# Kernel tuning notes

Hardware: AMD Instinct MI355X
Metric: run time of the kernel (lower is better)

Reference implementation:

```python
import jax, jax.numpy as jnp
import numpy as np

R = 4          # num_roles
L = 2          # num_layers
DIN = 128      # input/hidden feature dim
DOUT = 40     # output classes
N = 40000      # nodes
E = 480000     # edges


def setup_inputs() -> dict:
    key = jax.random.key(0)
    ks = jax.random.split(key, 12)
    x = jax.random.normal(ks[0], (N, R + DIN), dtype=jnp.float32)
    edge_index = jax.random.randint(ks[1], (2, E), 0, N, dtype=jnp.int64)
    s = 0.05
    Wm = jax.random.normal(ks[2], (L, R, DIN, DIN), dtype=jnp.float32) * s
    bm = jax.random.normal(ks[3], (L, R, DIN), dtype=jnp.float32) * s
    Wa = jax.random.normal(ks[4], (L, R, 2 * DIN, DIN), dtype=jnp.float32) * s
    ba = jax.random.normal(ks[5], (L, R, DIN), dtype=jnp.float32) * s
    W1 = jax.random.normal(ks[6], (DIN, DIN), dtype=jnp.float32) * s
    b1 = jax.random.normal(ks[7], (DIN,), dtype=jnp.float32) * s
    W2 = jax.random.normal(ks[8], (DIN, DOUT), dtype=jnp.float32) * s
    b2 = jax.random.normal(ks[9], (DOUT,), dtype=jnp.float32) * s
    return {"x": x, "edge_index": edge_index, "Wm": Wm, "bm": bm,
            "Wa": Wa, "ba": ba, "W1": W1, "b1": b1, "W2": W2, "b2": b2}


def _role_coef(roles):
    # Faithful to the original loop bug: linears[0] applied twice with roles[:,0],
    # linears[r] with roles[:,r] for r=1..R-2, linears[R-1] unused.
    return jnp.concatenate(
        [2.0 * roles[:, :1], roles[:, 1:R - 1], jnp.zeros_like(roles[:, :1])], axis=1)


def _graphsage_layer(xfull, src, dst, Wm_l, bm_l, Wa_l, ba_l):
    roles = xfull[:, :R]          # [N, R]
    feats = xfull[:, R:]          # [N, D]
    # --- message: gather source nodes, per-role linear + weighted sum, relu ---
    xr = roles[src]               # [E, R]
    xf = feats[src]               # [E, D]
    coef = _role_coef(xr)         # [E, R]
    lin = jnp.einsum('ei,rio->ero', xf, Wm_l) + bm_l[None]   # [E, R, O]
    msg = jax.nn.relu(jnp.einsum('er,ero->eo', coef, lin))    # [E, O]
    # --- aggregate: scatter-mean to target nodes ---
    ssum = jax.ops.segment_sum(msg, dst, num_segments=N)      # [N, O]
    cnt = jax.ops.segment_sum(jnp.ones((msg.shape[0], 1), msg.dtype), dst,
                              num_segments=N)                 # [N, 1]
    aggr = jnp.where(cnt > 0, ssum / jnp.maximum(cnt, 1.0), 0.0)
    # --- update: concat, per-role linear + weighted sum, relu, L2 normalize ---
    cat = jnp.concatenate([feats, aggr], axis=1)              # [N, D+O]
    coefn = _role_coef(roles)                                 # [N, R]
    lin2 = jnp.einsum('ni,rio->nro', cat, Wa_l) + ba_l[None]  # [N, R, O]
    out = jax.nn.relu(jnp.einsum('nr,nro->no', coefn, lin2))  # [N, O]
    norm = jnp.linalg.norm(out, axis=1, keepdims=True)
    return out / jnp.maximum(norm, 1e-12)


def reference(x, edge_index, Wm, bm, Wa, ba, W1, b1, W2, b2):
    src = edge_index[0]
    dst = edge_index[1]
    h = x
    for l in range(L):
        feats = _graphsage_layer(h, src, dst, Wm[l], bm[l], Wa[l], ba[l])
        feats = jax.nn.relu(feats)  # extra relu from GNNStack (dropout is identity in eval)
        h = jnp.concatenate([h[:, :R], feats], axis=1)
    z = h[:, R:]
    z = z @ W1 + b1               # post_mp linear 1 (dropout identity)
    logits = z @ W2 + b2          # post_mp linear 2
    return jax.nn.log_softmax(logits, axis=1)
```

## Files before the change

kernel.cpp:

```cpp
#include <hip/hip_runtime.h>
#include <hip/hip_fp16.h>

#define RN 4
#define XSTRIDE 132

typedef float    frag_cd __attribute__((ext_vector_type(4)));
typedef _Float16 frag_h  __attribute__((ext_vector_type(8)));

__global__ void count_kernel(const int* __restrict__ ei, int E, int* __restrict__ cnt) {
    int e = blockIdx.x * 256 + threadIdx.x;
    if (e < E) atomicAdd(&cnt[ei[E + e]], 1);
}

__global__ void scanA(const int* __restrict__ cnt, int N, int* __restrict__ bsums) {
    __shared__ int s[256];
    int t = threadIdx.x, n = blockIdx.x * 256 + t;
    s[t] = (n < N) ? cnt[n] : 0;
    __syncthreads();
    for (int off = 128; off > 0; off >>= 1) {
        if (t < off) s[t] += s[t + off];
        __syncthreads();
    }
    if (t == 0) bsums[blockIdx.x] = s[0];
}

__global__ void scanB(int* __restrict__ bsums, int nb) {
    __shared__ int s[256];
    int t = threadIdx.x;
    int v = (t < nb) ? bsums[t] : 0;
    s[t] = v; __syncthreads();
    for (int off = 1; off < 256; off <<= 1) {
        int add = (t >= off) ? s[t - off] : 0;
        __syncthreads();
        s[t] += add;
        __syncthreads();
    }
    if (t < nb) bsums[t] = s[t] - v;
}

__global__ void scanC(const int* __restrict__ cnt, int N,
                      const int* __restrict__ bsums, int* __restrict__ offs) {
    __shared__ int s[256];
    int t = threadIdx.x, n = blockIdx.x * 256 + t;
    int v = (n < N) ? cnt[n] : 0;
    s[t] = v; __syncthreads();
    for (int off = 1; off < 256; off <<= 1) {
        int add = (t >= off) ? s[t - off] : 0;
        __syncthreads();
        s[t] += add;
        __syncthreads();
    }
    if (n < N) {
        offs[n] = bsums[blockIdx.x] + s[t] - v;
        if (n == N - 1) offs[N] = bsums[blockIdx.x] + s[t];
    }
}

__global__ void fill_kernel(const int* __restrict__ ei, int E,
                            const int* __restrict__ offs, int* __restrict__ fc,
                            int* __restrict__ csr) {
    int e = blockIdx.x * 256 + threadIdx.x;
    if (e < E) {
        int dst = ei[E + e];
        int p = offs[dst] + atomicAdd(&fc[dst], 1);
        csr[p] = ei[e];
    }
}

#define CW_M  (6 * 128 * 128)
#define CW_A  (6 * 128 * 256)
#define CW_1  (128 * 128)
#define CW_2  (48 * 128)
__global__ void conv_all(const float* __restrict__ Wm, const float* __restrict__ Wa,
                         const float* __restrict__ W1, const float* __restrict__ W2,
                         _Float16* __restrict__ WmT, _Float16* __restrict__ WaT,
                         _Float16* __restrict__ W1T, _Float16* __restrict__ W2T) {
    int id = blockIdx.x * 256 + threadIdx.x;
    if (id < CW_M) {
        const int K = 128;
        int per = K * 128;
        int lr = id / per;  int l = lr / 3, r = lr - l * 3;
        int rem = id - lr * per;
        int k = rem >> 7, col = rem & 127;
        WmT[((size_t)lr * 128 + col) * K + k] =
            (_Float16)Wm[(((size_t)l * 4 + r) * K + k) * 128 + col];
    } else if (id < CW_M + CW_A) {
        int j = id - CW_M;
        const int K = 256;
        int per = K * 128;
        int lr = j / per;  int l = lr / 3, r = lr - l * 3;
        int rem = j - lr * per;
        int k = rem >> 7, col = rem & 127;
        WaT[((size_t)lr * 128 + col) * K + k] =
            (_Float16)Wa[(((size_t)l * 4 + r) * K + k) * 128 + col];
    } else if (id < CW_M + CW_A + CW_1) {
        int j = id - CW_M - CW_A;
        int col = j >> 7, k = j & 127;
        W1T[j] = (_Float16)W1[k * 128 + col];
    } else if (id < CW_M + CW_A + CW_1 + CW_2) {
        int j = id - CW_M - CW_A - CW_1;
        int col = j >> 7, k = j & 127;
        W2T[j] = (_Float16)((col < 40) ? W2[k * 40 + col] : 0.0f);
    }
}

__global__ void conv_x(const float* __restrict__ x, _Float16* __restrict__ X, int total) {
    int id = blockIdx.x * 256 + threadIdx.x;
    if (id >= total) return;
    int n = id >> 7, k = id & 127;
    X[id] = (_Float16)x[(size_t)n * XSTRIDE + RN + k];
}

__global__ __launch_bounds__(256) void agg_kernel(
    const int* __restrict__ csr, const int* __restrict__ offs,
    const _Float16* __restrict__ Mb, _Float16* __restrict__ S, int N)
{
    int node = blockIdx.x * 8 + (threadIdx.x >> 5);
    int lane = threadIdx.x & 31;
    if (node >= N) return;
    int lo = offs[node], hi = offs[node + 1];
    const uint2* M2 = (const uint2*)Mb;
    float a0 = 0.f, a1 = 0.f, a2 = 0.f, a3 = 0.f;
    int e = lo;
    for (; e + 3 < hi; e += 4) {
        #pragma unroll
        for (int j = 0; j < 4; ++j) {
            uint2 u = M2[(size_t)csr[e + j] * 32 + lane];
            float2 f0 = __half22float2(*(const __half2*)&u.x);
            float2 f1 = __half22float2(*(const __half2*)&u.y);
            a0 += f0.x; a1 += f0.y; a2 += f1.x; a3 += f1.y;
        }
    }
    for (; e < hi; ++e) {
        uint2 u = M2[(size_t)csr[e] * 32 + lane];
        float2 f0 = __half22float2(*(const __half2*)&u.x);
        float2 f1 = __half22float2(*(const __half2*)&u.y);
        a0 += f0.x; a1 += f0.y; a2 += f1.x; a3 += f1.y;
    }
    float inv = (hi > lo) ? 1.0f / (float)(hi - lo) : 0.0f;
    __half2 h0 = __float22half2_rn(make_float2(a0 * inv, a1 * inv));
    __half2 h1 = __float22half2_rn(make_float2(a2 * inv, a3 * inv));
    uint2 st; st.x = *(const uint*)&h0; st.y = *(const uint*)&h1;
    ((uint2*)S)[(size_t)node * 32 + lane] = st;
}

template<int KV, bool NORM>
__global__ __launch_bounds__(256) void gemm_mfma(
    const float* __restrict__ x,
    const _Float16* __restrict__ Fp,
    const _Float16* __restrict__ Sp,
    const _Float16* __restrict__ W,
    const float* __restrict__ bias,
    _Float16* __restrict__ out)
{
    __shared__ float cc[64][3];
    __shared__ float red[64][4];

    const int tid = threadIdx.x;
    const int n0 = blockIdx.x * 64;
    const int lane = tid & 63;
    const int wv = tid >> 6;
    const int q = lane >> 4;
    const int lb = lane & 15;
    const int w32 = wv * 32;

    if (tid < 64) {
        const float* xr = x + (size_t)(n0 + tid) * XSTRIDE;
        cc[tid][0] = 2.0f * xr[0];
        cc[tid][1] = xr[1];
        cc[tid][2] = xr[2];
    }
    __syncthreads();

    _Float16 ch16[4][3];
    #pragma unroll
    for (int nt = 0; nt < 4; ++nt)
        #pragma unroll
        for (int r = 0; r < 3; ++r)
            ch16[nt][r] = (_Float16)cc[nt * 16 + lb][r];

    frag_cd acc[4][2];
    #pragma unroll
    for (int nt = 0; nt < 4; ++nt)
        #pragma unroll
        for (int ct = 0; ct < 2; ++ct)
            acc[nt][ct] = (frag_cd){0.f, 0.f, 0.f, 0.f};

    size_t wrow[3][2];
    #pragma unroll
    for (int r = 0; r < 3; ++r)
        #pragma unroll
        for (int ct = 0; ct < 2; ++ct)
            wrow[r][ct] = ((size_t)(r * 128 + w32 + ct * 16 + lb)) * KV + q * 8;

    size_t arow[4];
    #pragma unroll
    for (int nt = 0; nt < 4; ++nt)
        arow[nt] = (size_t)(n0 + nt * 16 + lb) * 128 + q * 8;

    const int NCH = KV / 32;
    frag_h aF[3][4], bF[3][6];

    auto loadChunk = [&](int c, int buf) {
        const _Float16* ap; int kofs;
        if (KV == 128 || c < 4) { ap = Fp; kofs = c * 32; }
        else                    { ap = Sp; kofs = (c - 4) * 32; }
        #pragma unroll
        for (int nt = 0; nt < 4; ++nt)
            aF[buf][nt] = *(const frag_h*)(ap + arow[nt] + kofs);
        #pragma unroll
        for (int r = 0; r < 3; ++r)
            #pragma unroll
            for (int ct = 0; ct < 2; ++ct)
                bF[buf][r * 2 + ct] = *(const frag_h*)(W + wrow[r][ct] + c * 32);
    };

    loadChunk(0, 0);
    loadChunk(1, 1);

    #pragma unroll
    for (int ch = 0; ch < NCH; ++ch) {
        if (ch + 2 < NCH) loadChunk(ch + 2, (ch + 2) % 3);
        const int cur = ch % 3;
        #pragma unroll
        for (int r = 0; r < 3; ++r) {
            #pragma unroll
            for (int nt = 0; nt < 4; ++nt) {
                frag_h sa = aF[cur][nt] * ch16[nt][r];
                #pragma unroll
                for (int ct = 0; ct < 2; ++ct)
                    acc[nt][ct] = __builtin_amdgcn_mfma_f32_16x16x32_f16(
                        sa, bF[cur][r * 2 + ct], acc[nt][ct], 0, 0, 0);
            }
        }
    }

    float vv[4][2][4];
    #pragma unroll
    for (int ct = 0; ct < 2; ++ct) {
        int col = w32 + ct * 16 + lb;
        float b0 = bias[col], b1 = bias[128 + col], b2 = bias[256 + col];
        #pragma unroll
        for (int nt = 0; nt < 4; ++nt) {
            #pragma unroll
            for (int rg = 0; rg < 4; ++rg) {
                int row = nt * 16 + q * 4 + rg;
                float v = acc[nt][ct][rg]
                        + cc[row][0] * b0 + cc[row][1] * b1 + cc[row][2] * b2;
                vv[nt][ct][rg] = fmaxf(v, 0.0f);
            }
        }
    }

    if (NORM) {
        #pragma unroll
        for (int nt = 0; nt < 4; ++nt) {
            #pragma unroll
            for (int rg = 0; rg < 4; ++rg) {
                float ss = vv[nt][0][rg] * vv[nt][0][rg] + vv[nt][1][rg] * vv[nt][1][rg];
                #pragma unroll
                for (int m = 1; m < 16; m <<= 1) ss += __shfl_xor(ss, m, 64);
                if (lb == 0) red[nt * 16 + q * 4 + rg][wv] = ss;
            }
        }
        __syncthreads();
        #pragma unroll
        for (int nt = 0; nt < 4; ++nt) {
            #pragma unroll
            for (int rg = 0; rg < 4; ++rg) {
                int row = nt * 16 + q * 4 + rg;
                float t = red[row][0] + red[row][1] + red[row][2] + red[row][3];
                float inv = 1.0f / fmaxf(sqrtf(t), 1e-12f);
                #pragma unroll
                for (int ct = 0; ct < 2; ++ct) {
                    int col = w32 + ct * 16 + lb;
                    out[(size_t)(n0 + row) * 128 + col] = (_Float16)(vv[nt][ct][rg] * inv);
                }
            }
        }
    } else {
        #pragma unroll
        for (int nt = 0; nt < 4; ++nt)
            #pragma unroll
            for (int ct = 0; ct < 2; ++ct)
                #pragma unroll
                for (int rg = 0; rg < 4; ++rg) {
                    int row = nt * 16 + q * 4 + rg;
                    int col = w32 + ct * 16 + lb;
                    out[(size_t)(n0 + row) * 128 + col] = (_Float16)vv[nt][ct][rg];
                }
    }
}

__global__ __launch_bounds__(256) void final_mfma(
    const _Float16* __restrict__ F2,
    const _Float16* __restrict__ W1T,
    const float* __restrict__ b1,
    const _Float16* __restrict__ W2T,
    const float* __restrict__ b2,
    float* __restrict__ out)
{
    __shared__ _Float16 Z[64][136];

    const int tid = threadIdx.x;
    const int n0 = blockIdx.x * 64;
    const int lane = tid & 63;
    const int wv = tid >> 6;
    const int q = lane >> 4;
    const int lb = lane & 15;
    const int w32 = wv * 32;

    frag_cd acc[4][2];
    #pragma unroll
    for (int nt = 0; nt < 4; ++nt)
        #pragma unroll
        for (int ct = 0; ct < 2; ++ct) acc[nt][ct] = (frag_cd){0.f, 0.f, 0.f, 0.f};

    #pragma unroll
    for (int ch = 0; ch < 4; ++ch) {
        frag_h aF[4];
        #pragma unroll
        for (int nt = 0; nt < 4; ++nt)
            aF[nt] = *(const frag_h*)(F2 + (size_t)(n0 + nt * 16 + lb) * 128 + ch * 32 + q * 8);
        #pragma unroll
        for (int ct = 0; ct < 2; ++ct) {
            frag_h bF = *(const frag_h*)(W1T + (size_t)(w32 + ct * 16 + lb) * 128 + ch * 32 + q * 8);
            #pragma unroll
            for (int nt = 0; nt < 4; ++nt)
                acc[nt][ct] = __builtin_amdgcn_mfma_f32_16x16x32_f16(aF[nt], bF, acc[nt][ct], 0, 0, 0);
        }
    }
    #pragma unroll
    for (int ct = 0; ct < 2; ++ct) {
        int col = w32 + ct * 16 + lb;
        float bb = b1[col];
        #pragma unroll
        for (int nt = 0; nt < 4; ++nt)
            #pragma unroll
            for (int rg = 0; rg < 4; ++rg)
                Z[nt * 16 + q * 4 + rg][col] = (_Float16)(acc[nt][ct][rg] + bb);
    }
    __syncthreads();

    frag_cd a2[3];
    #pragma unroll
    for (int ct = 0; ct < 3; ++ct) a2[ct] = (frag_cd){0.f, 0.f, 0.f, 0.f};
    #pragma unroll
    for (int ch = 0; ch < 4; ++ch) {
        frag_h zF = *(const frag_h*)&Z[wv * 16 + lb][ch * 32 + q * 8];
        #pragma unroll
        for (int ct = 0; ct < 3; ++ct) {
            frag_h bF = *(const frag_h*)(W2T + (size_t)(ct * 16 + lb) * 128 + ch * 32 + q * 8);
            a2[ct] = __builtin_amdgcn_mfma_f32_16x16x32_f16(zF, bF, a2[ct], 0, 0, 0);
        }
    }

    float lg[3][4];
    #pragma unroll
    for (int ct = 0; ct < 3; ++ct) {
        int col = ct * 16 + lb;
        bool valid = col < 40;
        float bb = valid ? b2[col] : -1e30f;
        #pragma unroll
        for (int rg = 0; rg < 4; ++rg)
            lg[ct][rg] = valid ? (a2[ct][rg] + bb) : -1e30f;
    }
    #pragma unroll
    for (int rg = 0; rg < 4; ++rg) {
        float mx = fmaxf(fmaxf(lg[0][rg], lg[1][rg]), lg[2][rg]);
        #pragma unroll
        for (int m = 1; m < 16; m <<= 1) mx = fmaxf(mx, __shfl_xor(mx, m, 64));
        float sm = __expf(lg[0][rg] - mx) + __expf(lg[1][rg] - mx) + __expf(lg[2][rg] - mx);
        #pragma unroll
        for (int m = 1; m < 16; m <<= 1) sm += __shfl_xor(sm, m, 64);
        float ls = mx + __logf(sm);
        int row = n0 + wv * 16 + q * 4 + rg;
        #pragma unroll
        for (int ct = 0; ct < 3; ++ct) {
            int col = ct * 16 + lb;
            if (col < 40) out[(size_t)row * 40 + col] = lg[ct][rg] - ls;
        }
    }
}

extern "C" void kernel_launch(void* const* d_in, const int* in_sizes, int n_in,
                              void* d_out, int out_size, void* d_ws, size_t ws_size,
                              hipStream_t stream) {
    const float* x  = (const float*)d_in[0];
    const int*   ei = (const int*)d_in[1];
    const float* Wm = (const float*)d_in[2];
    const float* bm = (const float*)d_in[3];
    const float* Wa = (const float*)d_in[4];
    const float* ba = (const float*)d_in[5];
    const float* W1 = (const float*)d_in[6];
    const float* b1 = (const float*)d_in[7];
    const float* W2 = (const float*)d_in[8];
    const float* b2 = (const float*)d_in[9];
    float* out = (float*)d_out;

    const int N = in_sizes[0] / XSTRIDE;
    const int E = in_sizes[1] / 2;
    const int NB = (N + 255) / 256;
    const size_t P = (size_t)N * 128;

    _Float16* Mb  = (_Float16*)d_ws;
    _Float16* X   = Mb + P;
    _Float16* S   = X + P;
    _Float16* F1  = S + P;
    _Float16* WmT = F1 + P;
    _Float16* WaT = WmT + CW_M;
    _Float16* W1T = WaT + CW_A;
    _Float16* W2T = W1T + CW_1;
    int* cnt   = (int*)(W2T + CW_2);
    int* fc    = cnt + N;
    int* offs  = fc + N;
    int* csr   = offs + N + 1;
    int* bsums = csr + E;

    conv_all<<<(CW_M + CW_A + CW_1 + CW_2 + 255) / 256, 256, 0, stream>>>(
        Wm, Wa, W1, W2, WmT, WaT, W1T, W2T);
    conv_x<<<(N * 128 + 255) / 256, 256, 0, stream>>>(x, X, N * 128);

    hipMemsetAsync(cnt, 0, (size_t)2 * N * sizeof(int), stream);
    count_kernel<<<(E + 255) / 256, 256, 0, stream>>>(ei, E, cnt);
    scanA<<<NB, 256, 0, stream>>>(cnt, N, bsums);
    scanB<<<1, 256, 0, stream>>>(bsums, NB);
    scanC<<<NB, 256, 0, stream>>>(cnt, N, bsums, offs);
    fill_kernel<<<(E + 255) / 256, 256, 0, stream>>>(ei, E, offs, fc, csr);

    const int gblk = N / 64;
    for (int l = 0; l < 2; ++l) {
        const _Float16* fp = (l == 0) ? X : F1;
        _Float16* o = (l == 0) ? F1 : X;

        gemm_mfma<128, false><<<gblk, 256, 0, stream>>>(
            x, fp, nullptr,
            WmT + (size_t)l * 3 * 128 * 128, bm + (size_t)l * 4 * 128, Mb);
        agg_kernel<<<(N + 7) / 8, 256, 0, stream>>>(csr, offs, Mb, S, N);
        gemm_mfma<256, true><<<gblk, 256, 0, stream>>>(
            x, fp, S,
            WaT + (size_t)l * 3 * 128 * 256, ba + (size_t)l * 4 * 128, o);
    }

    final_mfma<<<N / 64, 256, 0, stream>>>(X, W1T, b1, W2T, b2, out);
}
```

Before: 307.5 us.

## Fuse prep kernels, drop scanB, widen agg loads, fully preload K=128 GEMM

Merges weight conversion, x conversion (now vectorised float4->half) and edge counting into a single prep kernel. It drops the separate scanB launch by having each scanC block reduce the preceding block sums itself. The aggregation kernel now uses 16 lanes per node with 16-byte loads instead of 32 lanes with 8-byte loads. The K=128 GEMM loads all fragments up front instead of using a rolling triple buffer. Together these cut launch count and per-load overhead, at the cost of more registers in the GEMM and redundant block-sum reductions in scanC.

```diff
diff --git a/kernel.cpp b/kernel.cpp
--- a/kernel.cpp
+++ b/kernel.cpp
@@ -6,75 +6,21 @@
 
 typedef float    frag_cd __attribute__((ext_vector_type(4)));
 typedef _Float16 frag_h  __attribute__((ext_vector_type(8)));
-
-__global__ void count_kernel(const int* __restrict__ ei, int E, int* __restrict__ cnt) {
-    int e = blockIdx.x * 256 + threadIdx.x;
-    if (e < E) atomicAdd(&cnt[ei[E + e]], 1);
-}
-
-__global__ void scanA(const int* __restrict__ cnt, int N, int* __restrict__ bsums) {
-    __shared__ int s[256];
-    int t = threadIdx.x, n = blockIdx.x * 256 + t;
-    s[t] = (n < N) ? cnt[n] : 0;
-    __syncthreads();
-    for (int off = 128; off > 0; off >>= 1) {
-        if (t < off) s[t] += s[t + off];
-        __syncthreads();
-    }
-    if (t == 0) bsums[blockIdx.x] = s[0];
-}
-
-__global__ void scanB(int* __restrict__ bsums, int nb) {
-    __shared__ int s[256];
-    int t = threadIdx.x;
-    int v = (t < nb) ? bsums[t] : 0;
-    s[t] = v; __syncthreads();
-    for (int off = 1; off < 256; off <<= 1) {
-        int add = (t >= off) ? s[t - off] : 0;
-        __syncthreads();
-        s[t] += add;
-        __syncthreads();
-    }
-    if (t < nb) bsums[t] = s[t] - v;
-}
-
-__global__ void scanC(const int* __restrict__ cnt, int N,
-                      const int* __restrict__ bsums, int* __restrict__ offs) {
-    __shared__ int s[256];
-    int t = threadIdx.x, n = blockIdx.x * 256 + t;
-    int v = (n < N) ? cnt[n] : 0;
-    s[t] = v; __syncthreads();
-    for (int off = 1; off < 256; off <<= 1) {
-        int add = (t >= off) ? s[t - off] : 0;
-        __syncthreads();
-        s[t] += add;
-        __syncthreads();
-    }
-    if (n < N) {
-        offs[n] = bsums[blockIdx.x] + s[t] - v;
-        if (n == N - 1) offs[N] = bsums[blockIdx.x] + s[t];
-    }
-}
-
-__global__ void fill_kernel(const int* __restrict__ ei, int E,
-                            const int* __restrict__ offs, int* __restrict__ fc,
-                            int* __restrict__ csr) {
-    int e = blockIdx.x * 256 + threadIdx.x;
-    if (e < E) {
-        int dst = ei[E + e];
-        int p = offs[dst] + atomicAdd(&fc[dst], 1);
-        csr[p] = ei[e];
-    }
-}
 
 #define CW_M  (6 * 128 * 128)
 #define CW_A  (6 * 128 * 256)
 #define CW_1  (128 * 128)
 #define CW_2  (48 * 128)
-__global__ void conv_all(const float* __restrict__ Wm, const float* __restrict__ Wa,
-                         const float* __restrict__ W1, const float* __restrict__ W2,
-                         _Float16* __restrict__ WmT, _Float16* __restrict__ WaT,
-                         _Float16* __restrict__ W1T, _Float16* __restrict__ W2T) {
+#define CW_TOT (CW_M + CW_A + CW_1 + CW_2)
+
+__global__ void prep_kernel(
+    const float* __restrict__ Wm, const float* __restrict__ Wa,
+    const float* __restrict__ W1, const float* __restrict__ W2,
+    _Float16* __restrict__ WmT, _Float16* __restrict__ WaT,
+    _Float16* __restrict__ W1T, _Float16* __restrict__ W2T,
+    const float* __restrict__ x, _Float16* __restrict__ X,
+    const int* __restrict__ ei, int* __restrict__ cnt, int N, int E)
+{
     int id = blockIdx.x * 256 + threadIdx.x;
     if (id < CW_M) {
         const int K = 128;
@@ -84,64 +30,141 @@
         int k = rem >> 7, col = rem & 127;
         WmT[((size_t)lr * 128 + col) * K + k] =
             (_Float16)Wm[(((size_t)l * 4 + r) * K + k) * 128 + col];
-    } else if (id < CW_M + CW_A) {
-        int j = id - CW_M;
+        return;
+    }
+    id -= CW_M;
+    if (id < CW_A) {
         const int K = 256;
         int per = K * 128;
-        int lr = j / per;  int l = lr / 3, r = lr - l * 3;
-        int rem = j - lr * per;
+        int lr = id / per;  int l = lr / 3, r = lr - l * 3;
+        int rem = id - lr * per;
         int k = rem >> 7, col = rem & 127;
         WaT[((size_t)lr * 128 + col) * K + k] =
             (_Float16)Wa[(((size_t)l * 4 + r) * K + k) * 128 + col];
-    } else if (id < CW_M + CW_A + CW_1) {
-        int j = id - CW_M - CW_A;
-        int col = j >> 7, k = j & 127;
-        W1T[j] = (_Float16)W1[k * 128 + col];
-    } else if (id < CW_M + CW_A + CW_1 + CW_2) {
-        int j = id - CW_M - CW_A - CW_1;
-        int col = j >> 7, k = j & 127;
-        W2T[j] = (_Float16)((col < 40) ? W2[k * 40 + col] : 0.0f);
-    }
-}
-
-__global__ void conv_x(const float* __restrict__ x, _Float16* __restrict__ X, int total) {
-    int id = blockIdx.x * 256 + threadIdx.x;
-    if (id >= total) return;
-    int n = id >> 7, k = id & 127;
-    X[id] = (_Float16)x[(size_t)n * XSTRIDE + RN + k];
+        return;
+    }
+    id -= CW_A;
+    if (id < CW_1) {
+        int col = id >> 7, k = id & 127;
+        W1T[id] = (_Float16)W1[k * 128 + col];
+        return;
+    }
+    id -= CW_1;
+    if (id < CW_2) {
+        int col = id >> 7, k = id & 127;
+        W2T[id] = (_Float16)((col < 40) ? W2[k * 40 + col] : 0.0f);
+        return;
+    }
+    id -= CW_2;
+    if (id < N * 16) {
+        int n = id >> 4, g = id & 15;
+        const float4* src = (const float4*)(x + (size_t)n * XSTRIDE + RN + g * 8);
+        float4 f0 = src[0], f1 = src[1];
+        __half2 h0 = __float22half2_rn(make_float2(f0.x, f0.y));
+        __half2 h1 = __float22half2_rn(make_float2(f0.z, f0.w));
+        __half2 h2 = __float22half2_rn(make_float2(f1.x, f1.y));
+        __half2 h3 = __float22half2_rn(make_float2(f1.z, f1.w));
+        uint4 st; st.x = *(uint*)&h0; st.y = *(uint*)&h1;
+        st.z = *(uint*)&h2; st.w = *(uint*)&h3;
+        ((uint4*)X)[(size_t)n * 16 + g] = st;
+        return;
+    }
+    id -= N * 16;
+    if (id < E) atomicAdd(&cnt[ei[E + id]], 1);
+}
+
+__global__ void scanA(const int* __restrict__ cnt, int N, int* __restrict__ bsums) {
+    __shared__ int s[256];
+    int t = threadIdx.x, n = blockIdx.x * 256 + t;
+    s[t] = (n < N) ? cnt[n] : 0;
+    __syncthreads();
+    for (int off = 128; off > 0; off >>= 1) {
+        if (t < off) s[t] += s[t + off];
+        __syncthreads();
+    }
+    if (t == 0) bsums[blockIdx.x] = s[0];
+}
+
+__global__ void scanC(const int* __restrict__ cnt, int N, int nb,
+                      const int* __restrict__ bsums, int* __restrict__ offs) {
+    __shared__ int s[256];
+    __shared__ int basebuf[256];
+    int t = threadIdx.x, n = blockIdx.x * 256 + t;
+    int bid = blockIdx.x;
+    basebuf[t] = (t < bid && t < nb) ? bsums[t] : 0;
+    __syncthreads();
+    for (int off = 128; off > 0; off >>= 1) {
+        if (t < off) basebuf[t] += basebuf[t + off];
+        __syncthreads();
+    }
+    int base = basebuf[0];
+    int v = (n < N) ? cnt[n] : 0;
+    s[t] = v; __syncthreads();
+    for (int off = 1; off < 256; off <<= 1) {
+        int add = (t >= off) ? s[t - off] : 0;
+        __syncthreads();
+        s[t] += add;
+        __syncthreads();
+    }
+    if (n < N) {
+        offs[n] = base + s[t] - v;
+        if (n == N - 1) offs[N] = base + s[t];
+    }
+}
+
+__global__ void fill_kernel(const int* __restrict__ ei, int E,
+                            const int* __restrict__ offs, int* __restrict__ fc,
+                            int* __restrict__ csr) {
+    int e = blockIdx.x * 256 + threadIdx.x;
+    if (e < E) {
+        int dst = ei[E + e];
+        int p = offs[dst] + atomicAdd(&fc[dst], 1);
+        csr[p] = ei[e];
+    }
 }
 
 __global__ __launch_bounds__(256) void agg_kernel(
     const int* __restrict__ csr, const int* __restrict__ offs,
     const _Float16* __restrict__ Mb, _Float16* __restrict__ S, int N)
 {
-    int node = blockIdx.x * 8 + (threadIdx.x >> 5);
-    int lane = threadIdx.x & 31;
+    int node = blockIdx.x * 16 + (threadIdx.x >> 4);
+    int lane = threadIdx.x & 15;
     if (node >= N) return;
     int lo = offs[node], hi = offs[node + 1];
-    const uint2* M2 = (const uint2*)Mb;
-    float a0 = 0.f, a1 = 0.f, a2 = 0.f, a3 = 0.f;
+    const uint4* M4 = (const uint4*)Mb;
+    float a[8];
+    #pragma unroll
+    for (int i = 0; i < 8; ++i) a[i] = 0.0f;
     int e = lo;
     for (; e + 3 < hi; e += 4) {
         #pragma unroll
         for (int j = 0; j < 4; ++j) {
-            uint2 u = M2[(size_t)csr[e + j] * 32 + lane];
+            uint4 u = M4[(size_t)csr[e + j] * 16 + lane];
             float2 f0 = __half22float2(*(const __half2*)&u.x);
             float2 f1 = __half22float2(*(const __half2*)&u.y);
-            a0 += f0.x; a1 += f0.y; a2 += f1.x; a3 += f1.y;
+            float2 f2 = __half22float2(*(const __half2*)&u.z);
+            float2 f3 = __half22float2(*(const __half2*)&u.w);
+            a[0] += f0.x; a[1] += f0.y; a[2] += f1.x; a[3] += f1.y;
+            a[4] += f2.x; a[5] += f2.y; a[6] += f3.x; a[7] += f3.y;
         }
     }
     for (; e < hi; ++e) {
-        uint2 u = M2[(size_t)csr[e] * 32 + lane];
+        uint4 u = M4[(size_t)csr[e] * 16 + lane];
         float2 f0 = __half22float2(*(const __half2*)&u.x);
         float2 f1 = __half22float2(*(const __half2*)&u.y);
-        a0 += f0.x; a1 += f0.y; a2 += f1.x; a3 += f1.y;
+        float2 f2 = __half22float2(*(const __half2*)&u.z);
+        float2 f3 = __half22float2(*(const __half2*)&u.w);
+        a[0] += f0.x; a[1] += f0.y; a[2] += f1.x; a[3] += f1.y;
+        a[4] += f2.x; a[5] += f2.y; a[6] += f3.x; a[7] += f3.y;
     }
     float inv = (hi > lo) ? 1.0f / (float)(hi - lo) : 0.0f;
-    __half2 h0 = __float22half2_rn(make_float2(a0 * inv, a1 * inv));
-    __half2 h1 = __float22half2_rn(make_float2(a2 * inv, a3 * inv));
-    uint2 st; st.x = *(const uint*)&h0; st.y = *(const uint*)&h1;
-    ((uint2*)S)[(size_t)node * 32 + lane] = st;
+    __half2 h0 = __float22half2_rn(make_float2(a[0] * inv, a[1] * inv));
+    __half2 h1 = __float22half2_rn(make_float2(a[2] * inv, a[3] * inv));
+    __half2 h2 = __float22half2_rn(make_float2(a[4] * inv, a[5] * inv));
+    __half2 h3 = __float22half2_rn(make_float2(a[6] * inv, a[7] * inv));
+    uint4 st; st.x = *(uint*)&h0; st.y = *(uint*)&h1;
+    st.z = *(uint*)&h2; st.w = *(uint*)&h3;
+    ((uint4*)S)[(size_t)node * 16 + lane] = st;
 }
 
 template<int KV, bool NORM>
@@ -198,40 +221,63 @@
     for (int nt = 0; nt < 4; ++nt)
         arow[nt] = (size_t)(n0 + nt * 16 + lb) * 128 + q * 8;
 
-    const int NCH = KV / 32;
-    frag_h aF[3][4], bF[3][6];
-
-    auto loadChunk = [&](int c, int buf) {
-        const _Float16* ap; int kofs;
-        if (KV == 128 || c < 4) { ap = Fp; kofs = c * 32; }
-        else                    { ap = Sp; kofs = (c - 4) * 32; }
-        #pragma unroll
-        for (int nt = 0; nt < 4; ++nt)
-            aF[buf][nt] = *(const frag_h*)(ap + arow[nt] + kofs);
-        #pragma unroll
-        for (int r = 0; r < 3; ++r)
-            #pragma unroll
-            for (int ct = 0; ct < 2; ++ct)
-                bF[buf][r * 2 + ct] = *(const frag_h*)(W + wrow[r][ct] + c * 32);
-    };
-
-    loadChunk(0, 0);
-    loadChunk(1, 1);
-
-    #pragma unroll
-    for (int ch = 0; ch < NCH; ++ch) {
-        if (ch + 2 < NCH) loadChunk(ch + 2, (ch + 2) % 3);
-        const int cur = ch % 3;
-        #pragma unroll
-        for (int r = 0; r < 3; ++r) {
-            #pragma unroll
-            for (int nt = 0; nt < 4; ++nt) {
-                frag_h sa = aF[cur][nt] * ch16[nt][r];
+    if (KV == 128) {
+        frag_h aF[4][4], bF[4][6];
+        #pragma unroll
+        for (int c = 0; c < 4; ++c) {
+            #pragma unroll
+            for (int nt = 0; nt < 4; ++nt)
+                aF[c][nt] = *(const frag_h*)(Fp + arow[nt] + c * 32);
+            #pragma unroll
+            for (int r = 0; r < 3; ++r)
                 #pragma unroll
                 for (int ct = 0; ct < 2; ++ct)
-                    acc[nt][ct] = __builtin_amdgcn_mfma_f32_16x16x32_f16(
-                        sa, bF[cur][r * 2 + ct], acc[nt][ct], 0, 0, 0);
-            }
+                    bF[c][r * 2 + ct] = *(const frag_h*)(W + wrow[r][ct] + c * 32);
+        }
+        #pragma unroll
+        for (int c = 0; c < 4; ++c)
+            #pragma unroll
+            for (int r = 0; r < 3; ++r)
+                #pragma unroll
+                for (int nt = 0; nt < 4; ++nt) {
+                    frag_h sa = aF[c][nt] * ch16[nt][r];
+                    #pragma unroll
+                    for (int ct = 0; ct < 2; ++ct)
+                        acc[nt][ct] = __builtin_amdgcn_mfma_f32_16x16x32_f16(
+                            sa, bF[c][r * 2 + ct], acc[nt][ct], 0, 0, 0);
+                }
+    } else {
+        const int NCH = KV / 32;
+        frag_h aF[3][4], bF[3][6];
+        auto loadChunk = [&](int c, int buf) {
+            const _Float16* ap; int kofs;
+            if (c < 4) { ap = Fp; kofs = c * 32; }
+            else       { ap = Sp; kofs = (c - 4) * 32; }
+            #pragma unroll
+            for (int nt = 0; nt < 4; ++nt)
+                aF[buf][nt] = *(const frag_h*)(ap + arow[nt] + kofs);
+            #pragma unroll
+            for (int r = 0; r < 3; ++r)
+                #pragma unroll
+                for (int ct = 0; ct < 2; ++ct)
+                    bF[buf][r * 2 + ct] = *(const frag_h*)(W + wrow[r][ct] + c * 32);
+        };
+        loadChunk(0, 0);
+        loadChunk(1, 1);
+        #pragma unroll
+        for (int ch = 0; ch < NCH; ++ch) {
+            if (ch + 2 < NCH) loadChunk(ch + 2, (ch + 2) % 3);
+            const int cur = ch % 3;
+            #pragma unroll
+            for (int r = 0; r < 3; ++r)
+                #pragma unroll
+                for (int nt = 0; nt < 4; ++nt) {
+                    frag_h sa = aF[cur][nt] * ch16[nt][r];
+                    #pragma unroll
+                    for (int ct = 0; ct < 2; ++ct)
+                        acc[nt][ct] = __builtin_amdgcn_mfma_f32_16x16x32_f16(
+                            sa, bF[cur][r * 2 + ct], acc[nt][ct], 0, 0, 0);
+                }
         }
     }
 
@@ -417,15 +463,13 @@
     int* csr   = offs + N + 1;
     int* bsums = csr + E;
 
-    conv_all<<<(CW_M + CW_A + CW_1 + CW_2 + 255) / 256, 256, 0, stream>>>(
-        Wm, Wa, W1, W2, WmT, WaT, W1T, W2T);
-    conv_x<<<(N * 128 + 255) / 256, 256, 0, stream>>>(x, X, N * 128);
-
     hipMemsetAsync(cnt, 0, (size_t)2 * N * sizeof(int), stream);
-    count_kernel<<<(E + 255) / 256, 256, 0, stream>>>(ei, E, cnt);
+    const int prep_total = CW_TOT + N * 16 + E;
+    prep_kernel<<<(prep_total + 255) / 256, 256, 0, stream>>>(
+        Wm, Wa, W1, W2, WmT, WaT, W1T, W2T, x, X, ei, cnt, N, E);
+
     scanA<<<NB, 256, 0, stream>>>(cnt, N, bsums);
-    scanB<<<1, 256, 0, stream>>>(bsums, NB);
-    scanC<<<NB, 256, 0, stream>>>(cnt, N, bsums, offs);
+    scanC<<<NB, 256, 0, stream>>>(cnt, N, NB, bsums, offs);
     fill_kernel<<<(E + 255) / 256, 256, 0, stream>>>(ei, E, offs, fc, csr);
 
     const int gblk = N / 64;
@@ -436,7 +480,7 @@
         gemm_mfma<128, false><<<gblk, 256, 0, stream>>>(
             x, fp, nullptr,
             WmT + (size_t)l * 3 * 128 * 128, bm + (size_t)l * 4 * 128, Mb);
-        agg_kernel<<<(N + 7) / 8, 256, 0, stream>>>(csr, offs, Mb, S, N);
+        agg_kernel<<<(N + 15) / 16, 256, 0, stream>>>(csr, offs, Mb, S, N);
         gemm_mfma<256, true><<<gblk, 256, 0, stream>>>(
             x, fp, S,
             WaT + (size_t)l * 3 * 128 * 256, ba + (size_t)l * 4 * 128, o);
```

Measured after the change: 295.9 us. 1.04x faster.
